# Kernel optimization log

Hardware: AMD Instinct MI355X
Metric: run time of the kernel (lower is better)

Reference implementation:

```python
import jax, jax.numpy as jnp
import numpy as np
from jax import lax

B, N, D, H, K = 8, 1024, 384, 6, 7
HD = D // H
EPS = 1e-5


def layer_norm(x, g, b):
    m = jnp.mean(x, axis=-1, keepdims=True)
    v = jnp.mean(jnp.square(x - m), axis=-1, keepdims=True)
    return (x - m) * lax.rsqrt(v + EPS) * g + b


def setup_inputs() -> dict:
    key = jax.random.key(0)
    ks = jax.random.split(key, 12)
    s = 0.02
    return {
        "x": jax.random.normal(ks[0], (B, N, D), jnp.float32),
        "qkv_w": jax.random.normal(ks[1], (3 * D, D), jnp.float32) * s,
        "qkv_b": jnp.zeros((3 * D,), jnp.float32),
        "proj_w": jax.random.normal(ks[2], (D, D), jnp.float32) * s,
        "proj_b": jnp.zeros((D,), jnp.float32),
        "t_before": jnp.eye(H, dtype=jnp.float32) + jax.random.normal(ks[3], (H, H), jnp.float32) * 0.01,
        "t_after": jnp.eye(H, dtype=jnp.float32) + jax.random.normal(ks[4], (H, H), jnp.float32) * 0.01,
        "dw_w": jax.random.normal(ks[5], (D, 1, K), jnp.float32) * s,
        "dw_b": jnp.zeros((D,), jnp.float32),
        "mlp_ln_g": jnp.ones((D,), jnp.float32),
        "mlp_ln_b": jnp.zeros((D,), jnp.float32),
        "norm1_g": jnp.ones((D,), jnp.float32),
        "norm1_b": jnp.zeros((D,), jnp.float32),
        "norm2_g": jnp.ones((D,), jnp.float32),
        "norm2_b": jnp.zeros((D,), jnp.float32),
        "fc1_w": jax.random.normal(ks[6], (4 * D, D), jnp.float32) * s,
        "fc1_b": jnp.zeros((4 * D,), jnp.float32),
        "fc2_w": jax.random.normal(ks[7], (D, 4 * D), jnp.float32) * s,
        "fc2_b": jnp.zeros((D,), jnp.float32),
    }


def reference(x, qkv_w, qkv_b, proj_w, proj_b, t_before, t_after, dw_w, dw_b,
              mlp_ln_g, mlp_ln_b, norm1_g, norm1_b, norm2_g, norm2_b,
              fc1_w, fc1_b, fc2_w, fc2_b):
    # ---- attention branch ----
    h = layer_norm(x, norm1_g, norm1_b)
    qkv = h @ qkv_w.T + qkv_b                                  # (B,N,3D)
    qkv = qkv.reshape(B, N, 3, H, HD).transpose(2, 0, 3, 1, 4)  # (3,B,H,N,hd)
    q, k, v = qkv[0], qkv[1], qkv[2]
    scale = HD ** -0.5
    scores = jnp.einsum('bhnd,bhmd->bhnm', q, k) * scale        # (B,H,N,N)
    scores = jnp.einsum('gh,bhnm->bgnm', t_before, scores)       # head-mix pre-softmax
    probs = jax.nn.softmax(scores, axis=-1)
    probs = jnp.einsum('gh,bhnm->bgnm', t_after, probs)          # head-mix post-softmax
    attn_out = jnp.einsum('bhnm,bhmd->bhnd', probs, v)           # (B,H,N,hd)
    attn_out = attn_out.transpose(0, 2, 1, 3).reshape(B, N, D)
    attn_out = attn_out @ proj_w.T + proj_b
    x = x + attn_out
    # ---- MLP branch ----
    h = layer_norm(x, norm2_g, norm2_b)
    # depthwise conv1d over tokens: (B,D,N), groups=D, same padding
    h_t = h.transpose(0, 2, 1)
    h_t = lax.conv_general_dilated(h_t, dw_w, window_strides=(1,),
                                   padding=[(K // 2, K // 2)],
                                   dimension_numbers=('NCH', 'OIH', 'NCH'),
                                   feature_group_count=D)
    h = h_t.transpose(0, 2, 1) + dw_b
    h = layer_norm(h, mlp_ln_g, mlp_ln_b)
    h = jax.nn.gelu(h @ fc1_w.T + fc1_b, approximate=False)
    h = h @ fc2_w.T + fc2_b
    return x + h
```

## Files before the change

kernel.cpp:

```cpp
#include <hip/hip_runtime.h>
#include <hip/hip_bf16.h>

#define BB 8
#define NN 1024
#define DD 384
#define HH 6
#define HD 64
#define BN 8192
#define D3 1152
#define D4 1536
#define SEC 3145728

typedef __attribute__((ext_vector_type(8))) short short8;
typedef __attribute__((ext_vector_type(4))) float f32x4;
typedef __attribute__((ext_vector_type(2))) float f32x2;

typedef __attribute__((address_space(3))) unsigned char as3_byte;
typedef __attribute__((address_space(1))) const unsigned char as1_byte;

__device__ __forceinline__ void gload16(const void* g, void* l){
  __builtin_amdgcn_global_load_lds((as1_byte*)g, (as3_byte*)l, 16, 0, 0);
}

__device__ __forceinline__ float b2f(unsigned short u){
  union{unsigned int i; float f;} x; x.i=((unsigned int)u)<<16; return x.f;
}
__device__ __forceinline__ unsigned short f2b(float f){
  unsigned int u=__float_as_uint(f);
  return (unsigned short)((u + 0x7FFFu + ((u>>16)&1u))>>16);
}

__global__ void cvt_kernel(const float* __restrict__ w0, const float* __restrict__ w1,
                           const float* __restrict__ w2, const float* __restrict__ w3,
                           unsigned short* __restrict__ out){
  int i = blockIdx.x*256 + threadIdx.x;
  float v;
  if (i < 442368)        v = w0[i];
  else if (i < 589824)   v = w1[i - 442368];
  else if (i < 1179648)  v = w2[i - 589824];
  else if (i < 1769472)  v = w3[i - 1179648];
  else return;
  out[i] = f2b(v);
}

template<int OUTBF>
__global__ __launch_bounds__(128)
void ln_kernel(const float* __restrict__ in, const float* __restrict__ gg, const float* __restrict__ bb,
               float* __restrict__ outf, unsigned short* __restrict__ outb){
  int row = blockIdx.x, t = threadIdx.x;
  const float* r = in + (size_t)row*DD;
  float v0=r[t], v1=r[t+128], v2=r[t+256];
  float s=v0+v1+v2, q=v0*v0+v1*v1+v2*v2;
  #pragma unroll
  for (int o=32;o>0;o>>=1){ s+=__shfl_down(s,o); q+=__shfl_down(q,o); }
  __shared__ float ls[2], lq[2];
  if ((t&63)==0){ ls[t>>6]=s; lq[t>>6]=q; }
  __syncthreads();
  float S=ls[0]+ls[1], Q=lq[0]+lq[1];
  float mean=S*(1.0f/DD);
  float rstd=rsqrtf(Q*(1.0f/DD)-mean*mean+1e-5f);
  float o0=(v0-mean)*rstd*gg[t]+bb[t];
  float o1=(v1-mean)*rstd*gg[t+128]+bb[t+128];
  float o2=(v2-mean)*rstd*gg[t+256]+bb[t+256];
  if (OUTBF){ unsigned short* o=outb+(size_t)row*DD; o[t]=f2b(o0); o[t+128]=f2b(o1); o[t+256]=f2b(o2); }
  else      { float* o=outf+(size_t)row*DD; o[t]=o0; o[t+128]=o1; o[t+256]=o2; }
}

__global__ __launch_bounds__(128)
void conv_ln_kernel(const float* __restrict__ h2, const float* __restrict__ dww, const float* __restrict__ dwb,
                    const float* __restrict__ gg, const float* __restrict__ bb, unsigned short* __restrict__ out){
  int row=blockIdx.x, t=threadIdx.x;
  int bi=row>>10, n=row&1023;
  const float* base = h2 + (size_t)(bi<<10)*DD;
  float a[3];
  #pragma unroll
  for (int j=0;j<3;j++){
    int d=t+j*128;
    float acc=dwb[d];
    #pragma unroll
    for (int k=0;k<7;k++){
      int nn=n+k-3;
      if (nn>=0 && nn<NN) acc += dww[d*7+k]*base[(size_t)nn*DD + d];
    }
    a[j]=acc;
  }
  float s=a[0]+a[1]+a[2], q=a[0]*a[0]+a[1]*a[1]+a[2]*a[2];
  #pragma unroll
  for (int o=32;o>0;o>>=1){ s+=__shfl_down(s,o); q+=__shfl_down(q,o); }
  __shared__ float ls[2], lq[2];
  if ((t&63)==0){ ls[t>>6]=s; lq[t>>6]=q; }
  __syncthreads();
  float S=ls[0]+ls[1], Q=lq[0]+lq[1];
  float mean=S*(1.0f/DD);
  float rstd=rsqrtf(Q*(1.0f/DD)-mean*mean+1e-5f);
  unsigned short* o = out + (size_t)row*DD;
  #pragma unroll
  for (int j=0;j<3;j++){
    int d=t+j*128;
    o[d]=f2b((a[j]-mean)*rstd*gg[d]+bb[d]);
  }
}

template<int MODE, int TN>
__global__ __launch_bounds__(256)
void gemm_kernel(const unsigned short* __restrict__ A, const unsigned short* __restrict__ W,
                 const float* __restrict__ bias, const float* __restrict__ resid,
                 float* __restrict__ outf, unsigned short* __restrict__ outb,
                 int Kdim, int Ncols){
  constexpr int JF = TN/32;
  __shared__ __align__(16) unsigned short lds_a[2][128*32];
  __shared__ __align__(16) unsigned short lds_b[2][TN*32];
  int t=threadIdx.x, lane=t&63, w=t>>6;
  int bm = blockIdx.x*128;
  int bn = blockIdx.y*TN;
  int wr = w>>1, wc = w&1;
  int rm = lane&15, r16 = lane>>4;
  f32x4 acc[4][JF] = {};
  char* ldsa_c = (char*)lds_a;
  char* ldsb_c = (char*)lds_b;
  int abyte[4], bbyte[JF];
  #pragma unroll
  for (int i=0;i<4;i++){
    int ra = wr*64 + i*16 + rm;
    abyte[i] = ra*64 + ((r16 ^ ((ra>>1)&3))*16);
  }
  #pragma unroll
  for (int j=0;j<JF;j++){
    int rb = wc*(TN/2) + j*16 + rm;
    bbyte[j] = rb*64 + ((r16 ^ ((rb>>1)&3))*16);
  }
  auto stage = [&](int buf, int k0){
    #pragma unroll
    for (int c=0;c<2;c++){
      int u = t + c*256;
      int row = u>>2, sl = (u&3) ^ ((row>>1)&3);
      gload16(A + (size_t)(bm+row)*Kdim + k0 + sl*8, ldsa_c + buf*8192 + u*16);
    }
    #pragma unroll
    for (int c=0;c<TN/64;c++){
      int u = t + c*256;
      int row = u>>2, sl = (u&3) ^ ((row>>1)&3);
      gload16(W + (size_t)(bn+row)*Kdim + k0 + sl*8, ldsb_c + buf*(TN*64) + u*16);
    }
  };
  int niter = Kdim>>5;
  stage(0, 0);
  __syncthreads();
  for (int it=0; it<niter; ++it){
    if (it+1<niter) stage((it+1)&1, (it+1)<<5);
    int ab = (it&1)*8192, bb2 = (it&1)*(TN*64);
    short8 af[4], bf[JF];
    #pragma unroll
    for (int i=0;i<4;i++) af[i]=*reinterpret_cast<const short8*>(ldsa_c + ab + abyte[i]);
    #pragma unroll
    for (int j=0;j<JF;j++) bf[j]=*reinterpret_cast<const short8*>(ldsb_c + bb2 + bbyte[j]);
    #pragma unroll
    for (int i=0;i<4;i++)
      #pragma unroll
      for (int j=0;j<JF;j++)
        acc[i][j]=__builtin_amdgcn_mfma_f32_16x16x32_bf16(af[i],bf[j],acc[i][j],0,0,0);
    __syncthreads();
  }
  #pragma unroll
  for (int i=0;i<4;i++){
    #pragma unroll
    for (int j=0;j<JF;j++){
      #pragma unroll
      for (int r=0;r<4;r++){
        int row = bm + wr*64 + i*16 + r16*4 + r;
        int col = bn + wc*(TN/2) + j*16 + rm;
        float v = acc[i][j][r] + bias[col];
        if (MODE==0){
          int c = col/384; int rem = col - c*384; int hh = rem>>6, d = rem&63;
          if (c==0) v *= 0.125f;
          int bi = row>>10, nn = row&1023;
          outb[(size_t)c*SEC + (((size_t)(bi*6+hh))<<16) + (nn<<6) + d] = f2b(v);
        } else if (MODE==1){
          size_t idx = (size_t)row*Ncols + col;
          outf[idx] = resid[idx] + v;
        } else {
          float ge = 0.5f*v*(1.0f+erff(v*0.70710678118654752f));
          outb[(size_t)row*Ncols + col] = f2b(ge);
        }
      }
    }
  }
}

__global__ __launch_bounds__(256)
void vt8_kernel(const unsigned short* __restrict__ V, unsigned char* __restrict__ V8){
  __shared__ unsigned short tile[64][66];
  int z = blockIdx.y, m0 = blockIdx.x*64;
  int t = threadIdx.x, c = t&63, r4 = t>>6;
  #pragma unroll
  for (int p=0;p<16;p++){
    int m = r4 + p*4;
    tile[m][c] = V[((size_t)z<<16) + ((size_t)(m0+m)<<6) + c];
  }
  __syncthreads();
  #pragma unroll
  for (int p=0;p<16;p++){
    int d = r4 + p*4;
    float v = b2f(tile[c][d]);
    int pk = __builtin_amdgcn_cvt_pk_fp8_f32(v, v, 0, false);
    V8[((size_t)z<<16) + ((size_t)d<<10) + m0 + c] = (unsigned char)(pk & 0xff);
  }
}

__global__ __launch_bounds__(256, 2)
void smx_kernel(const unsigned short* __restrict__ qkv, const float* __restrict__ tbm,
                unsigned char* __restrict__ E, float* __restrict__ invl){
  __shared__ __align__(16) unsigned short Qs[6*16*64];
  __shared__ __align__(16) unsigned short Ks[6*64*64];
  __shared__ float lred[4][6][16];
  int t=threadIdx.x, lane=t&63, w=t>>6;
  int b = blockIdx.x&7, nt = blockIdx.x>>3;
  int n0 = nt*16;
  int c16 = lane&15, r16 = lane>>4;
  const unsigned short* kbase = qkv + SEC + (((size_t)(b*6))<<16);
  #pragma unroll
  for (int i=0;i<3;i++){
    int u = t + i*256;
    int r = u>>3, s = (u&7) ^ (r&7);
    int h = r>>4, n = r&15;
    gload16(qkv + (((size_t)(b*6+h))<<16) + ((size_t)(n0+n)<<6) + s*8,
            (char*)Qs + u*16);
  }
  auto stageK = [&](int m0){
    #pragma unroll
    for (int i=0;i<12;i++){
      int u = t + i*256;
      int r = u>>3, s = (u&7) ^ (r&7);
      int h = r>>6, m = r&63;
      gload16(kbase + (((size_t)h)<<16) + ((size_t)(m0+m)<<6) + s*8,
              (char*)Ks + u*16);
    }
  };
  stageK(0);
  float tbr[36];
  #pragma unroll
  for (int i=0;i<36;i++) tbr[i]=tbm[i]*1.44269504088896f;
  __syncthreads();
  int sw = c16&7;
  short8 qf[6][2];
  #pragma unroll
  for (int h=0;h<6;h++){
    int qb = (h*16 + c16)*128;
    qf[h][0] = *(const short8*)((char*)Qs + qb + ((r16^sw)<<4));
    qf[h][1] = *(const short8*)((char*)Qs + qb + (((4+r16)^sw)<<4));
  }
  int kb0 = (w*16 + c16)*128 + ((r16^sw)<<4);
  int kb1 = (w*16 + c16)*128 + (((4+r16)^sw)<<4);
  float lsum[6] = {0.f,0.f,0.f,0.f,0.f,0.f};
  for (int mt=0; mt<16; ++mt){
    int m0 = mt*64;
    f32x4 aq[6] = {};
    #pragma unroll
    for (int h=0;h<6;h++){
      short8 kf0 = *(const short8*)((char*)Ks + h*8192 + kb0);
      short8 kf1 = *(const short8*)((char*)Ks + h*8192 + kb1);
      aq[h] = __builtin_amdgcn_mfma_f32_16x16x32_bf16(kf0, qf[h][0], aq[h], 0,0,0);
      aq[h] = __builtin_amdgcn_mfma_f32_16x16x32_bf16(kf1, qf[h][1], aq[h], 0,0,0);
    }
    __syncthreads();
    if (mt<15) stageK(m0+64);
    float ef[6][4];
    #pragma unroll
    for (int r=0;r<4;r++){
      float s0=aq[0][r], s1=aq[1][r], s2=aq[2][r],
            s3=aq[3][r], s4=aq[4][r], s5=aq[5][r];
      #pragma unroll
      for (int g=0;g<6;g++){
        float sm = tbr[g*6]*s0 + tbr[g*6+1]*s1 + tbr[g*6+2]*s2
                 + tbr[g*6+3]*s3 + tbr[g*6+4]*s4 + tbr[g*6+5]*s5;
        float e = __builtin_amdgcn_exp2f(sm);
        ef[g][r] = e;
        lsum[g] += e;
      }
    }
    #pragma unroll
    for (int g=0;g<6;g++){
      int pkv = __builtin_amdgcn_cvt_pk_fp8_f32(ef[g][0], ef[g][1], 0, false);
      pkv = __builtin_amdgcn_cvt_pk_fp8_f32(ef[g][2], ef[g][3], pkv, true);
      *(unsigned int*)(E + (((size_t)(b*6+g))<<20) + ((size_t)(n0+c16)<<10) + m0 + w*16 + r16*4)
        = (unsigned int)pkv;
    }
    if (mt<15) __syncthreads();
  }
  #pragma unroll
  for (int g=0;g<6;g++){
    lsum[g] += __shfl_xor(lsum[g],16);
    lsum[g] += __shfl_xor(lsum[g],32);
  }
  if (r16==0){
    #pragma unroll
    for (int g=0;g<6;g++) lred[w][g][c16] = lsum[g];
  }
  __syncthreads();
  if (w==0 && r16==0){
    #pragma unroll
    for (int g=0;g<6;g++){
      float l = lred[0][g][c16]+lred[1][g][c16]+lred[2][g][c16]+lred[3][g][c16];
      invl[(((size_t)(b*6+g))<<10) + n0 + c16] = 256.0f/l;
    }
  }
}

__global__ __launch_bounds__(256, 2)
void pvmix_kernel(const unsigned char* __restrict__ E, const unsigned char* __restrict__ V8,
                  const float* __restrict__ invl, const float* __restrict__ tam,
                  unsigned short* __restrict__ outp){
  __shared__ __align__(16) unsigned char Es[6*16*64];
  __shared__ __align__(16) unsigned char Vs[6*64*64];
  __shared__ __align__(16) unsigned char pms[6*16*64];
  int t=threadIdx.x, lane=t&63, w=t>>6;
  int b = blockIdx.x&7, nt = blockIdx.x>>3;
  int n0 = nt*16;
  int c16 = lane&15, r16 = lane>>4;
  int mn = t&15, mg = (t>>4)&7, gh = t>>7;
  float cf[3][6];
  #pragma unroll
  for (int g=0;g<6;g++){
    float iv = invl[(((size_t)(b*6+g))<<10) + n0 + mn];
    #pragma unroll
    for (int j=0;j<3;j++) cf[j][g] = tam[(gh*3+j)*6 + g]*iv;
  }
  auto stageE = [&](int m0){
    #pragma unroll
    for (int i=0;i<2;i++){
      int u = t + i*256;
      if (u<384){
        int r = u>>2, s = (u&3) ^ (r&3);
        int g = r>>4, n = r&15;
        gload16(E + (((size_t)(b*6+g))<<20) + ((size_t)(n0+n)<<10) + m0 + s*16,
                (char*)Es + u*16);
      }
    }
  };
  auto stageV = [&](int m0){
    #pragma unroll
    for (int i=0;i<6;i++){
      int u = t + i*256;
      int r = u>>2, s = (u&3) ^ (r&3);
      int g = r>>6, d = r&63;
      gload16(V8 + (((size_t)(b*6+g))<<16) + ((size_t)d<<10) + m0 + s*16,
              (char*)Vs + u*16);
    }
  };
  stageE(0); stageV(0);
  __syncthreads();
  f32x4 acc[6] = {};
  for (int mt=0; mt<16; ++mt){
    float e[6][8];
    #pragma unroll
    for (int g=0;g<6;g++){
      int row = g*16 + mn;
      int byteo = row*64 + ((mg*8) ^ ((row&3)<<4));
      unsigned int lo = *(const unsigned int*)(Es + byteo);
      unsigned int hi = *(const unsigned int*)(Es + byteo + 4);
      f32x2 p0 = __builtin_amdgcn_cvt_pk_f32_fp8(lo, false);
      f32x2 p1 = __builtin_amdgcn_cvt_pk_f32_fp8(lo, true);
      f32x2 p2 = __builtin_amdgcn_cvt_pk_f32_fp8(hi, false);
      f32x2 p3 = __builtin_amdgcn_cvt_pk_f32_fp8(hi, true);
      e[g][0]=p0.x; e[g][1]=p0.y; e[g][2]=p1.x; e[g][3]=p1.y;
      e[g][4]=p2.x; e[g][5]=p2.y; e[g][6]=p3.x; e[g][7]=p3.y;
    }
    #pragma unroll
    for (int j=0;j<3;j++){
      float pm[8];
      #pragma unroll
      for (int m=0;m<8;m++)
        pm[m] = cf[j][0]*e[0][m]+cf[j][1]*e[1][m]+cf[j][2]*e[2][m]
              + cf[j][3]*e[3][m]+cf[j][4]*e[4][m]+cf[j][5]*e[5][m];
      int d0 = __builtin_amdgcn_cvt_pk_fp8_f32(pm[0], pm[1], 0, false);
      d0 = __builtin_amdgcn_cvt_pk_fp8_f32(pm[2], pm[3], d0, true);
      int d1 = __builtin_amdgcn_cvt_pk_fp8_f32(pm[4], pm[5], 0, false);
      d1 = __builtin_amdgcn_cvt_pk_fp8_f32(pm[6], pm[7], d1, true);
      int prow = (gh*3+j)*16 + mn;
      int pbyte = prow*64 + ((mg*8) ^ ((mn&7)<<3));
      *(unsigned int*)(pms + pbyte)     = (unsigned int)d0;
      *(unsigned int*)(pms + pbyte + 4) = (unsigned int)d1;
    }
    __syncthreads();
    if (mt<15) stageE((mt+1)*64);
    #pragma unroll
    for (int g=0;g<6;g++){
      int arow = g*16 + c16;
      int vrow = g*64 + w*16 + c16;
      #pragma unroll
      for (int kk=0;kk<2;kk++){
        long af = *(const long*)(pms + arow*64 + ((kk*32 + r16*8) ^ ((c16&7)<<3)));
        long bf = *(const long*)(Vs + vrow*64
                   + ((((kk*2 + (r16>>1)) ^ (vrow&3))<<4) + ((r16&1)<<3)));
        acc[g] = __builtin_amdgcn_mfma_f32_16x16x32_fp8_fp8(af, bf, acc[g], 0,0,0);
      }
    }
    __syncthreads();
    if (mt<15) stageV((mt+1)*64);
  }
  #pragma unroll
  for (int g=0;g<6;g++)
    #pragma unroll
    for (int r=0;r<4;r++){
      int n = n0 + r16*4 + r;
      int d = g*64 + w*16 + c16;
      outp[((size_t)(b*1024 + n))*DD + d] = f2b(acc[g][r] * 0.00390625f);
    }
}

extern "C" void kernel_launch(void* const* d_in, const int* in_sizes, int n_in,
                              void* d_out, int out_size, void* d_ws, size_t ws_size,
                              hipStream_t stream){
  const float* x      = (const float*)d_in[0];
  const float* qkv_w  = (const float*)d_in[1];
  const float* qkv_b  = (const float*)d_in[2];
  const float* proj_w = (const float*)d_in[3];
  const float* proj_b = (const float*)d_in[4];
  const float* t_before=(const float*)d_in[5];
  const float* t_after =(const float*)d_in[6];
  const float* dw_w   = (const float*)d_in[7];
  const float* dw_b   = (const float*)d_in[8];
  const float* mlp_g  = (const float*)d_in[9];
  const float* mlp_b  = (const float*)d_in[10];
  const float* n1_g   = (const float*)d_in[11];
  const float* n1_b   = (const float*)d_in[12];
  const float* n2_g   = (const float*)d_in[13];
  const float* n2_b   = (const float*)d_in[14];
  const float* fc1_w  = (const float*)d_in[15];
  const float* fc1_b  = (const float*)d_in[16];
  const float* fc2_w  = (const float*)d_in[17];
  const float* fc2_b  = (const float*)d_in[18];
  float* out = (float*)d_out;
  char* ws = (char*)d_ws;
  unsigned short* qkvwb = (unsigned short*)(ws + 0);
  unsigned short* projwb= (unsigned short*)(ws + 884736);
  unsigned short* fc1wb = (unsigned short*)(ws + 1179648);
  unsigned short* fc2wb = (unsigned short*)(ws + 2359296);
  unsigned short* hb    = (unsigned short*)(ws + 3538944);
  unsigned short* qkvb  = (unsigned short*)(ws + 9830400);
  unsigned char*  V8    = (unsigned char*) (ws + 28704768);
  unsigned char*  Ebuf  = (unsigned char*) (ws + 34996224);
  unsigned short* attnb = (unsigned short*)(ws + 85327872);
  float*          x2    = (float*)(ws + 91619328);
  float* invl = (float*)(ws + 8781824);
  float* h2 = (float*)qkvb;
  unsigned short* hcln = hb;
  unsigned short* fc1o = (unsigned short*)Ebuf;

  cvt_kernel<<<(1769472+255)/256,256,0,stream>>>(qkv_w, proj_w, fc1_w, fc2_w, qkvwb);

  ln_kernel<1><<<BN,128,0,stream>>>(x, n1_g, n1_b, nullptr, hb);
  { dim3 g(BN/128, D3/128); gemm_kernel<0,128><<<g,256,0,stream>>>(hb, qkvwb, qkv_b, nullptr, nullptr, qkvb, DD, D3); }
  { dim3 g(NN/64, 48); vt8_kernel<<<g,256,0,stream>>>(qkvb + 2*(size_t)SEC, V8); }
  smx_kernel<<<512,256,0,stream>>>(qkvb, t_before, Ebuf, invl);
  pvmix_kernel<<<512,256,0,stream>>>(Ebuf, V8, invl, t_after, attnb);
  { dim3 g(BN/128, DD/64); gemm_kernel<1,64><<<g,256,0,stream>>>(attnb, projwb, proj_b, x, x2, nullptr, DD, DD); }
  ln_kernel<0><<<BN,128,0,stream>>>(x2, n2_g, n2_b, h2, nullptr);
  conv_ln_kernel<<<BN,128,0,stream>>>(h2, dw_w, dw_b, mlp_g, mlp_b, hcln);
  { dim3 g(BN/128, D4/128); gemm_kernel<2,128><<<g,256,0,stream>>>(hcln, fc1wb, fc1_b, nullptr, nullptr, fc1o, DD, D4); }
  { dim3 g(BN/128, DD/64); gemm_kernel<1,64><<<g,256,0,stream>>>(fc1o, fc2wb, fc2_b, x2, out, nullptr, D4, DD); }
}
```

Baseline: 207.0 us.

## Fuse V fp8 transpose into QKV GEMM and split softmax over key halves

The QKV GEMM epilogue now writes V straight to the transposed fp8 layout, so the separate vt8 transpose kernel is removed. The softmax kernel is split across two key halves (1024 blocks instead of 512), and partial row sums are accumulated with atomicAdd into a buffer that cvt_kernel zeroes. The reciprocal moves into pvmix. MFMA sections are also given raised wave priority. The costs are atomic traffic, scattered byte stores from the GEMM epilogue, and a change in float summation order.

Result: no change. 208.0 us (+0.5%).

```diff
diff --git a/kernel.cpp b/kernel.cpp
--- a/kernel.cpp
+++ b/kernel.cpp
@@ -32,15 +32,13 @@
 
 __global__ void cvt_kernel(const float* __restrict__ w0, const float* __restrict__ w1,
                            const float* __restrict__ w2, const float* __restrict__ w3,
-                           unsigned short* __restrict__ out){
+                           unsigned short* __restrict__ out, float* __restrict__ lbuf){
   int i = blockIdx.x*256 + threadIdx.x;
-  float v;
-  if (i < 442368)        v = w0[i];
-  else if (i < 589824)   v = w1[i - 442368];
-  else if (i < 1179648)  v = w2[i - 589824];
-  else if (i < 1769472)  v = w3[i - 1179648];
-  else return;
-  out[i] = f2b(v);
+  if (i < 442368)        out[i] = f2b(w0[i]);
+  else if (i < 589824)   out[i] = f2b(w1[i - 442368]);
+  else if (i < 1179648)  out[i] = f2b(w2[i - 589824]);
+  else if (i < 1769472)  out[i] = f2b(w3[i - 1179648]);
+  else if (i < 1818624)  lbuf[i - 1769472] = 0.f;
 }
 
 template<int OUTBF>
@@ -106,6 +104,7 @@
 void gemm_kernel(const unsigned short* __restrict__ A, const unsigned short* __restrict__ W,
                  const float* __restrict__ bias, const float* __restrict__ resid,
                  float* __restrict__ outf, unsigned short* __restrict__ outb,
+                 unsigned char* __restrict__ v8out,
                  int Kdim, int Ncols){
   constexpr int JF = TN/32;
   __shared__ __align__(16) unsigned short lds_a[2][128*32];
@@ -172,9 +171,14 @@
         float v = acc[i][j][r] + bias[col];
         if (MODE==0){
           int c = col/384; int rem = col - c*384; int hh = rem>>6, d = rem&63;
-          if (c==0) v *= 0.125f;
           int bi = row>>10, nn = row&1023;
-          outb[(size_t)c*SEC + (((size_t)(bi*6+hh))<<16) + (nn<<6) + d] = f2b(v);
+          if (c==2){
+            int pk = __builtin_amdgcn_cvt_pk_fp8_f32(v, v, 0, false);
+            v8out[(((size_t)(bi*6+hh))<<16) + ((size_t)d<<10) + nn] = (unsigned char)(pk & 0xff);
+          } else {
+            if (c==0) v *= 0.125f;
+            outb[(size_t)c*SEC + (((size_t)(bi*6+hh))<<16) + (nn<<6) + d] = f2b(v);
+          }
         } else if (MODE==1){
           size_t idx = (size_t)row*Ncols + col;
           outf[idx] = resid[idx] + v;
@@ -187,35 +191,16 @@
   }
 }
 
-__global__ __launch_bounds__(256)
-void vt8_kernel(const unsigned short* __restrict__ V, unsigned char* __restrict__ V8){
-  __shared__ unsigned short tile[64][66];
-  int z = blockIdx.y, m0 = blockIdx.x*64;
-  int t = threadIdx.x, c = t&63, r4 = t>>6;
-  #pragma unroll
-  for (int p=0;p<16;p++){
-    int m = r4 + p*4;
-    tile[m][c] = V[((size_t)z<<16) + ((size_t)(m0+m)<<6) + c];
-  }
-  __syncthreads();
-  #pragma unroll
-  for (int p=0;p<16;p++){
-    int d = r4 + p*4;
-    float v = b2f(tile[c][d]);
-    int pk = __builtin_amdgcn_cvt_pk_fp8_f32(v, v, 0, false);
-    V8[((size_t)z<<16) + ((size_t)d<<10) + m0 + c] = (unsigned char)(pk & 0xff);
-  }
-}
-
 __global__ __launch_bounds__(256, 2)
 void smx_kernel(const unsigned short* __restrict__ qkv, const float* __restrict__ tbm,
-                unsigned char* __restrict__ E, float* __restrict__ invl){
+                unsigned char* __restrict__ E, float* __restrict__ lbuf){
   __shared__ __align__(16) unsigned short Qs[6*16*64];
   __shared__ __align__(16) unsigned short Ks[6*64*64];
   __shared__ float lred[4][6][16];
   int t=threadIdx.x, lane=t&63, w=t>>6;
-  int b = blockIdx.x&7, nt = blockIdx.x>>3;
-  int n0 = nt*16;
+  int blk = blockIdx.x;
+  int b = blk&7, nt = (blk>>3)&63, mh = blk>>9;
+  int n0 = nt*16, mbase = mh<<9;
   int c16 = lane&15, r16 = lane>>4;
   const unsigned short* kbase = qkv + SEC + (((size_t)(b*6))<<16);
   #pragma unroll
@@ -236,7 +221,7 @@
               (char*)Ks + u*16);
     }
   };
-  stageK(0);
+  stageK(mbase);
   float tbr[36];
   #pragma unroll
   for (int i=0;i<36;i++) tbr[i]=tbm[i]*1.44269504088896f;
@@ -252,9 +237,10 @@
   int kb0 = (w*16 + c16)*128 + ((r16^sw)<<4);
   int kb1 = (w*16 + c16)*128 + (((4+r16)^sw)<<4);
   float lsum[6] = {0.f,0.f,0.f,0.f,0.f,0.f};
-  for (int mt=0; mt<16; ++mt){
-    int m0 = mt*64;
+  for (int mt=0; mt<8; ++mt){
+    int m0 = mbase + mt*64;
     f32x4 aq[6] = {};
+    __builtin_amdgcn_s_setprio(1);
     #pragma unroll
     for (int h=0;h<6;h++){
       short8 kf0 = *(const short8*)((char*)Ks + h*8192 + kb0);
@@ -262,8 +248,9 @@
       aq[h] = __builtin_amdgcn_mfma_f32_16x16x32_bf16(kf0, qf[h][0], aq[h], 0,0,0);
       aq[h] = __builtin_amdgcn_mfma_f32_16x16x32_bf16(kf1, qf[h][1], aq[h], 0,0,0);
     }
+    __builtin_amdgcn_s_setprio(0);
     __syncthreads();
-    if (mt<15) stageK(m0+64);
+    if (mt<7) stageK(m0+64);
     float ef[6][4];
     #pragma unroll
     for (int r=0;r<4;r++){
@@ -285,7 +272,7 @@
       *(unsigned int*)(E + (((size_t)(b*6+g))<<20) + ((size_t)(n0+c16)<<10) + m0 + w*16 + r16*4)
         = (unsigned int)pkv;
     }
-    if (mt<15) __syncthreads();
+    if (mt<7) __syncthreads();
   }
   #pragma unroll
   for (int g=0;g<6;g++){
@@ -301,14 +288,14 @@
     #pragma unroll
     for (int g=0;g<6;g++){
       float l = lred[0][g][c16]+lred[1][g][c16]+lred[2][g][c16]+lred[3][g][c16];
-      invl[(((size_t)(b*6+g))<<10) + n0 + c16] = 256.0f/l;
+      atomicAdd(&lbuf[(((size_t)(b*6+g))<<10) + n0 + c16], l);
     }
   }
 }
 
 __global__ __launch_bounds__(256, 2)
 void pvmix_kernel(const unsigned char* __restrict__ E, const unsigned char* __restrict__ V8,
-                  const float* __restrict__ invl, const float* __restrict__ tam,
+                  const float* __restrict__ lbuf, const float* __restrict__ tam,
                   unsigned short* __restrict__ outp){
   __shared__ __align__(16) unsigned char Es[6*16*64];
   __shared__ __align__(16) unsigned char Vs[6*64*64];
@@ -321,7 +308,7 @@
   float cf[3][6];
   #pragma unroll
   for (int g=0;g<6;g++){
-    float iv = invl[(((size_t)(b*6+g))<<10) + n0 + mn];
+    float iv = 256.0f/lbuf[(((size_t)(b*6+g))<<10) + n0 + mn];
     #pragma unroll
     for (int j=0;j<3;j++) cf[j][g] = tam[(gh*3+j)*6 + g]*iv;
   }
@@ -439,24 +426,23 @@
   unsigned short* hb    = (unsigned short*)(ws + 3538944);
   unsigned short* qkvb  = (unsigned short*)(ws + 9830400);
   unsigned char*  V8    = (unsigned char*) (ws + 28704768);
+  float*          lbuf  = (float*)        (ws + 31850496);
   unsigned char*  Ebuf  = (unsigned char*) (ws + 34996224);
   unsigned short* attnb = (unsigned short*)(ws + 85327872);
   float*          x2    = (float*)(ws + 91619328);
-  float* invl = (float*)(ws + 8781824);
   float* h2 = (float*)qkvb;
   unsigned short* hcln = hb;
   unsigned short* fc1o = (unsigned short*)Ebuf;
 
-  cvt_kernel<<<(1769472+255)/256,256,0,stream>>>(qkv_w, proj_w, fc1_w, fc2_w, qkvwb);
+  cvt_kernel<<<7104,256,0,stream>>>(qkv_w, proj_w, fc1_w, fc2_w, qkvwb, lbuf);
 
   ln_kernel<1><<<BN,128,0,stream>>>(x, n1_g, n1_b, nullptr, hb);
-  { dim3 g(BN/128, D3/128); gemm_kernel<0,128><<<g,256,0,stream>>>(hb, qkvwb, qkv_b, nullptr, nullptr, qkvb, DD, D3); }
-  { dim3 g(NN/64, 48); vt8_kernel<<<g,256,0,stream>>>(qkvb + 2*(size_t)SEC, V8); }
-  smx_kernel<<<512,256,0,stream>>>(qkvb, t_before, Ebuf, invl);
-  pvmix_kernel<<<512,256,0,stream>>>(Ebuf, V8, invl, t_after, attnb);
-  { dim3 g(BN/128, DD/64); gemm_kernel<1,64><<<g,256,0,stream>>>(attnb, projwb, proj_b, x, x2, nullptr, DD, DD); }
+  { dim3 g(BN/128, D3/128); gemm_kernel<0,128><<<g,256,0,stream>>>(hb, qkvwb, qkv_b, nullptr, nullptr, qkvb, V8, DD, D3); }
+  smx_kernel<<<1024,256,0,stream>>>(qkvb, t_before, Ebuf, lbuf);
+  pvmix_kernel<<<512,256,0,stream>>>(Ebuf, V8, lbuf, t_after, attnb);
+  { dim3 g(BN/128, DD/64); gemm_kernel<1,64><<<g,256,0,stream>>>(attnb, projwb, proj_b, x, x2, nullptr, nullptr, DD, DD); }
   ln_kernel<0><<<BN,128,0,stream>>>(x2, n2_g, n2_b, h2, nullptr);
   conv_ln_kernel<<<BN,128,0,stream>>>(h2, dw_w, dw_b, mlp_g, mlp_b, hcln);
-  { dim3 g(BN/128, D4/128); gemm_kernel<2,128><<<g,256,0,stream>>>(hcln, fc1wb, fc1_b, nullptr, nullptr, fc1o, DD, D4); }
-  { dim3 g(BN/128, DD/64); gemm_kernel<1,64><<<g,256,0,stream>>>(fc1o, fc2wb, fc2_b, x2, out, nullptr, D4, DD); }
-}
+  { dim3 g(BN/128, D4/128); gemm_kernel<2,128><<<g,256,0,stream>>>(hcln, fc1wb, fc1_b, nullptr, nullptr, fc1o, nullptr, DD, D4); }
+  { dim3 g(BN/128, DD/64); gemm_kernel<1,64><<<g,256,0,stream>>>(fc1o, fc2wb, fc2_b, x2, out, nullptr, nullptr, D4, DD); }
+}
```
